# Kernel optimization log

Hardware: AMD Instinct MI355X
Metric: run time of the kernel (lower is better)

Reference implementation:

```python
import jax, jax.numpy as jnp
import numpy as np

B, N = 8, 2048
DIN, DH, DE = 32, 64, 64
R = 3          # number_relations
L = 3          # num_layers -> 1 first + 1 block + 1 last
PRED_IN = DH * (L - 1) + DE  # concat: 64*2 + 64 = 192
EPS_BN = 1e-5
EPS_NORM = 1e-12


def setup_inputs() -> dict:
    key = jax.random.key(0)
    ks = jax.random.split(key, 12)
    x = jax.random.normal(ks[0], (B, N, DIN), jnp.float32)
    # relation labels in {0..R}; 0 = no edge, 1..R = relation type
    relation = jax.random.randint(ks[1], (B, N, N), 0, R + 1).astype(jnp.int32)
    # adjacency is the 0/1 edge indicator (float), as the torch code treats it
    adj = (relation > 0).astype(jnp.float32)
    s = 0.05
    w_first = jax.random.normal(ks[2], (R, DIN, DH), jnp.float32) * s
    b_first = jnp.zeros((DH,), jnp.float32)
    w_block = jax.random.normal(ks[3], (R, DH, DH), jnp.float32) * s
    b_block = jnp.zeros((DH,), jnp.float32)
    w_last = jax.random.normal(ks[4], (R, DH, DE), jnp.float32) * s
    b_last = jnp.zeros((DE,), jnp.float32)
    w_map = jax.random.normal(ks[5], (PRED_IN, DE), jnp.float32) * s
    b_map = jnp.zeros((DE,), jnp.float32)
    return {"x": x, "relation": relation, "adj": adj,
            "w_first": w_first, "b_first": b_first,
            "w_block": w_block, "b_block": b_block,
            "w_last": w_last, "b_last": b_last,
            "w_map": w_map, "b_map": b_map}


def _graph_conv(x, rel, W, b):
    # rel: [B,N,N] (int labels or float adjacency); W: [R, din, dout]
    y = jnp.zeros((x.shape[0], x.shape[1], W.shape[2]), x.dtype)
    for i in range(R):  # fixed, small relation count
        mask = (rel == (i + 1)).astype(x.dtype)            # [B,N,N]
        h = jnp.einsum('bij,bjd->bid', mask, x)            # masked aggregation
        y = y + jnp.einsum('bid,de->bie', h, W[i])
    y = y + b
    # F.normalize(p=2, dim=2): v / max(||v||, eps)
    nrm = jnp.sqrt(jnp.sum(y * y, axis=2, keepdims=True))
    return y / jnp.maximum(nrm, EPS_NORM)


def _apply_bn(x):
    # fresh BatchNorm1d(N) in training mode, affine weight=1/bias=0:
    # normalize over (batch, feature) per node index, biased variance
    mean = jnp.mean(x, axis=(0, 2), keepdims=True)
    var = jnp.mean(jnp.square(x - mean), axis=(0, 2), keepdims=True)
    return (x - mean) * jax.lax.rsqrt(var + EPS_BN)


def reference(x, relation, adj, w_first, b_first, w_block, b_block,
              w_last, b_last, w_map, b_map):
    # conv_first uses `relation`
    h = _apply_bn(jax.nn.relu(_graph_conv(x, relation, w_first, b_first)))
    out_all = [jnp.max(h, axis=1)]
    # conv_block and conv_last are (faithfully) called with `adj` as relation
    h = _apply_bn(jax.nn.relu(_graph_conv(h, adj, w_block, b_block)))
    out_all.append(jnp.max(h, axis=1))
    h = _graph_conv(h, adj, w_last, b_last)
    out_all.append(jnp.max(h, axis=1))
    output = jnp.concatenate(out_all, axis=1)        # [B, PRED_IN]
    ypred = output @ w_map + b_map                   # map_model Linear
    return (output, ypred)
```

## Files before the change

kernel.cpp:

```cpp
#include <hip/hip_runtime.h>


#define NN 2048
#define PLANE_W 1048576L

typedef short short8 __attribute__((ext_vector_type(8)));
typedef float floatx4 __attribute__((ext_vector_type(4)));

__device__ __forceinline__ unsigned short f2bf(float x) {
  unsigned u = __float_as_uint(x);
  u += 0x7FFFu + ((u >> 16) & 1u);
  return (unsigned short)(u >> 16);
}

__device__ void dev_xw_first(char* smemc, int u, int tid,
                             const float* __restrict__ x,
                             const float* __restrict__ w,
                             unsigned short* __restrict__ xws) {
  float* xs = (float*)smemc;
  float* wsh = (float*)(smemc + 64 * 33 * 4);
  const int jc = u & 31, b = (u >> 5) & 7, r = u >> 8;
  const int j0 = jc * 64;
  for (int idx = tid; idx < 64 * 32; idx += 256) {
    int row = idx >> 5, f = idx & 31;
    xs[row * 33 + f] = x[((long)b * NN + j0 + row) * 32 + f];
    wsh[idx] = w[r * 2048 + idx];
  }
  __syncthreads();
  const int j = tid & 63, g = tid >> 6;
  const int k = j0 + j;
  const int kblk = k >> 5, kq = (k >> 3) & 3, kj = k & 7;
  unsigned short* dst =
      xws + (((long)(r * 8 + b) * 64 + kblk) * 4 + g) * 512 + kj;
  float xr[32];
#pragma unroll
  for (int f = 0; f < 32; ++f) xr[f] = xs[j * 33 + f];
#pragma unroll
  for (int ii = 0; ii < 16; ++ii) {
    float acc = 0.f;
#pragma unroll
    for (int f = 0; f < 32; ++f) acc += xr[f] * wsh[f * 64 + g * 16 + ii];
    dst[(kq * 16 + ii) * 8] = f2bf(acc);
  }
  __syncthreads();
}

__global__ __launch_bounds__(256) void k_pack_xw1(const int* __restrict__ rel,
                                                  unsigned* __restrict__ planes,
                                                  const float* __restrict__ x,
                                                  const float* __restrict__ w,
                                                  unsigned short* __restrict__ xws) {
  __shared__ __align__(16) char smem[16640];
  const int bid = blockIdx.x, tid = threadIdx.x;
  if (bid < 768) dev_xw_first(smem, bid, tid, x, w, xws);
  for (long t = (long)bid * 256 + tid; t < 1048576L; t += 4096L * 256) {
    int w32 = (int)(t & 63);
    long bi = t >> 6;
    const int4* rp = (const int4*)(rel + bi * NN + w32 * 32);
    unsigned m0 = 0, m1 = 0, m2 = 0;
#pragma unroll
    for (int c = 0; c < 8; ++c) {
      int4 v = rp[c];
      int vv[4] = {v.x, v.y, v.z, v.w};
#pragma unroll
      for (int j = 0; j < 4; ++j) {
        unsigned b1 = 1u << (c * 4 + j);
        m0 |= (vv[j] == 1) ? b1 : 0u;
        m1 |= (vv[j] == 2) ? b1 : 0u;
        m2 |= (vv[j] == 3) ? b1 : 0u;
      }
    }
    long o = bi * 64 + w32;
    planes[o] = m0;
    planes[PLANE_W + o] = m1;
    planes[2 * PLANE_W + o] = m2;
  }
}

template <int NREL, bool RELU, bool POOL3>
__global__ __launch_bounds__(512) void k_gemm8(
    const unsigned* __restrict__ planes, const unsigned short* __restrict__ xws,
    const float* __restrict__ bias, float* __restrict__ Hout,
    float* __restrict__ part3) {
  constexpr int SMEM = (NREL * 8448 > 16640) ? NREL * 8448 : 16640;
  __shared__ __align__(16) char smem[SMEM];
  unsigned* mw = (unsigned*)smem;
  floatx4* cb = (floatx4*)smem;
  const int bid = blockIdx.x;
  const int b = bid & 7, it = bid >> 3;
  const int tid = threadIdx.x;
  const int wave = tid >> 6, lane = tid & 63;
  const int m = lane & 15, kq = lane >> 4;
  const int i0 = it * 64;

  floatx4 acc[4][4];
#pragma unroll
  for (int rs = 0; rs < 4; ++rs)
#pragma unroll
    for (int t = 0; t < 4; ++t) acc[rs][t] = floatx4{0, 0, 0, 0};

  for (int chunk = 0; chunk < 2; ++chunk) {
    for (int idx = tid; idx < NREL * 2048; idx += 512) {
      int p = idx >> 11, rem = idx & 2047, row = rem >> 5, w = rem & 31;
      long g = ((long)b * NN + i0 + row) * 64 + chunk * 32 + w;
      unsigned v;
      if (NREL == 3)
        v = planes[(long)p * PLANE_W + g];
      else
        v = planes[g] | planes[PLANE_W + g] | planes[2 * PLANE_W + g];
      mw[(p * 64 + row) * 33 + w] = v;
    }
    __syncthreads();
#pragma unroll
    for (int j = 0; j < 4; ++j) {
      const int kk = j * 8 + wave;
      const int kblk = chunk * 32 + kk;
#pragma unroll
      for (int p = 0; p < NREL; ++p) {
        const unsigned short* bb =
            xws + ((long)(p * 8 + b) * 64 + kblk) * 2048 + lane * 8;
        short8 bf0 = *(const short8*)(bb);
        short8 bf1 = *(const short8*)(bb + 512);
        short8 bf2 = *(const short8*)(bb + 1024);
        short8 bf3 = *(const short8*)(bb + 1536);
#pragma unroll
        for (int rs = 0; rs < 4; ++rs) {
          unsigned word = mw[(p * 64 + rs * 16 + m) * 33 + kk];
          unsigned byte = (word >> (kq * 8)) & 0xffu;
          unsigned pp = byte | (byte << 15);
          union {
            unsigned uu[4];
            short8 s8;
          } fr;
          unsigned w0 = pp & 0x00010001u;
          fr.uu[0] = (w0 << 14) - (w0 << 7);
          unsigned w1 = pp & 0x00040004u;
          fr.uu[1] = (w1 << 12) - (w1 << 5);
          unsigned w2 = pp & 0x00100010u;
          fr.uu[2] = (w2 << 10) - (w2 << 3);
          unsigned w3 = pp & 0x00400040u;
          fr.uu[3] = (w3 << 8) - (w3 << 1);
          acc[rs][0] = __builtin_amdgcn_mfma_f32_16x16x32_bf16(fr.s8, bf0,
                                                              acc[rs][0], 0, 0, 0);
          acc[rs][1] = __builtin_amdgcn_mfma_f32_16x16x32_bf16(fr.s8, bf1,
                                                              acc[rs][1], 0, 0, 0);
          acc[rs][2] = __builtin_amdgcn_mfma_f32_16x16x32_bf16(fr.s8, bf2,
                                                              acc[rs][2], 0, 0, 0);
          acc[rs][3] = __builtin_amdgcn_mfma_f32_16x16x32_bf16(fr.s8, bf3,
                                                              acc[rs][3], 0, 0, 0);
        }
      }
    }
    __syncthreads();
  }

  for (int k = 7; k >= 1; --k) {
    if (wave == k) {
      if (k == 7) {
#pragma unroll
        for (int rs = 0; rs < 4; ++rs)
#pragma unroll
          for (int t = 0; t < 4; ++t) cb[(rs * 4 + t) * 64 + lane] = acc[rs][t];
      } else {
#pragma unroll
        for (int rs = 0; rs < 4; ++rs)
#pragma unroll
          for (int t = 0; t < 4; ++t) {
            floatx4 v = cb[(rs * 4 + t) * 64 + lane];
            cb[(rs * 4 + t) * 64 + lane] = v + acc[rs][t];
          }
      }
    }
    __syncthreads();
  }
  if (wave == 0) {
#pragma unroll
    for (int rs = 0; rs < 4; ++rs)
#pragma unroll
      for (int t = 0; t < 4; ++t) acc[rs][t] += cb[(rs * 4 + t) * 64 + lane];
    float bv[4];
#pragma unroll
    for (int t = 0; t < 4; ++t) bv[t] = bias[t * 16 + m];
    float pmt[4] = {-3.4e38f, -3.4e38f, -3.4e38f, -3.4e38f};
#pragma unroll
    for (int rs = 0; rs < 4; ++rs) {
      float ss[4];
#pragma unroll
      for (int reg = 0; reg < 4; ++reg) {
#pragma unroll
        for (int t = 0; t < 4; ++t) acc[rs][t][reg] += bv[t];
        ss[reg] = acc[rs][0][reg] * acc[rs][0][reg] +
                  acc[rs][1][reg] * acc[rs][1][reg] +
                  acc[rs][2][reg] * acc[rs][2][reg] +
                  acc[rs][3][reg] * acc[rs][3][reg];
#pragma unroll
        for (int off = 1; off <= 8; off <<= 1)
          ss[reg] += __shfl_xor(ss[reg], off);
        ss[reg] = 1.0f / fmaxf(sqrtf(ss[reg]), 1e-12f);
      }
#pragma unroll
      for (int t = 0; t < 4; ++t) {
#pragma unroll
        for (int reg = 0; reg < 4; ++reg) {
          float o = acc[rs][t][reg] * ss[reg];
          if (RELU) o = fmaxf(o, 0.0f);
          if (POOL3)
            pmt[t] = fmaxf(pmt[t], o);
          else
            Hout[((long)b * NN + i0 + rs * 16 + kq * 4 + reg) * 64 + t * 16 + m] = o;
        }
      }
    }
    if (POOL3) {
#pragma unroll
      for (int t = 0; t < 4; ++t) {
        pmt[t] = fmaxf(pmt[t], __shfl_xor(pmt[t], 16));
        pmt[t] = fmaxf(pmt[t], __shfl_xor(pmt[t], 32));
      }
      if (kq == 0) {
#pragma unroll
        for (int t = 0; t < 4; ++t)
          part3[((long)b * 32 + it) * 64 + t * 16 + m] = pmt[t];
      }
    }
  }
}

__global__ __launch_bounds__(256) void k_xwh_bn(const float* __restrict__ H,
                                                const float* __restrict__ w,
                                                unsigned short* __restrict__ xws,
                                                float* __restrict__ PP) {
  __shared__ float hs[64 * 65];
  __shared__ float wsh[64 * 64];
  __shared__ float sm[64], srs[64];
  const int bid = blockIdx.x, tid = threadIdx.x;
  const int jc = bid & 31, b = bid >> 5;
  const int j0 = jc * 64;
  {
    const int n = tid >> 2, q = tid & 3;
    float s1 = 0.f, s2 = 0.f;
#pragma unroll
    for (int bb = 0; bb < 8; ++bb) {
      const float4* hp =
          (const float4*)(H + ((long)bb * NN + j0 + n) * 64 + q * 16);
#pragma unroll
      for (int c = 0; c < 4; ++c) {
        float4 v = hp[c];
        s1 += v.x + v.y + v.z + v.w;
        s2 += v.x * v.x + v.y * v.y + v.z * v.z + v.w * v.w;
      }
    }
    s1 += __shfl_xor(s1, 1);
    s2 += __shfl_xor(s2, 1);
    s1 += __shfl_xor(s1, 2);
    s2 += __shfl_xor(s2, 2);
    if (q == 0) {
      float mean = s1 * (1.0f / 512.0f);
      float var = fmaxf(s2 * (1.0f / 512.0f) - mean * mean, 0.0f);
      sm[n] = mean;
      srs[n] = rsqrtf(var + 1e-5f);
    }
  }
  __syncthreads();
  for (int idx = tid; idx < 4096; idx += 256) {
    int row = idx >> 6, f = idx & 63;
    float v = H[((long)b * NN + j0 + row) * 64 + f];
    hs[row * 65 + f] = (v - sm[row]) * srs[row];
    wsh[idx] = w[idx];
  }
  __syncthreads();
  {
    const int j = tid & 63, g = tid >> 6;
    const int k = j0 + j;
    const int kblk = k >> 5, kq = (k >> 3) & 3, kj = k & 7;
    unsigned short* dst = xws + (((long)b * 64 + kblk) * 4 + g) * 512 + kj;
    float acc[16];
#pragma unroll
    for (int ii = 0; ii < 16; ++ii) acc[ii] = 0.f;
#pragma unroll
    for (int c = 0; c < 4; ++c) {
      float xr[16];
#pragma unroll
      for (int f = 0; f < 16; ++f) xr[f] = hs[j * 65 + c * 16 + f];
#pragma unroll
      for (int ii = 0; ii < 16; ++ii)
#pragma unroll
        for (int f = 0; f < 16; ++f)
          acc[ii] += xr[f] * wsh[(c * 16 + f) * 64 + g * 16 + ii];
    }
#pragma unroll
    for (int ii = 0; ii < 16; ++ii) dst[(kq * 16 + ii) * 8] = f2bf(acc[ii]);
  }
  if (b == 0) {
#pragma unroll
    for (int part = 0; part < 2; ++part) {
      const int col = part * 256 + tid;
      const int bb = col >> 6, e = col & 63;
      float mx = -3.4e38f;
      for (int n = 0; n < 64; ++n) {
        float v = H[((long)bb * NN + j0 + n) * 64 + e];
        mx = fmaxf(mx, (v - sm[n]) * srs[n]);
      }
      PP[(long)jc * 512 + col] = mx;
    }
  }
}

__global__ __launch_bounds__(512) void k_tail(const float* __restrict__ PP1,
                                              const float* __restrict__ PP2,
                                              const float* __restrict__ P3,
                                              float* __restrict__ out,
                                              const float* __restrict__ wmap,
                                              const float* __restrict__ bmap) {
  const int col = threadIdx.x;
  const int bb = col >> 6, e = col & 63;
  float m1 = -3.4e38f, m2 = -3.4e38f, m3 = -3.4e38f;
#pragma unroll
  for (int c = 0; c < 32; ++c) {
    m1 = fmaxf(m1, PP1[(long)c * 512 + col]);
    m2 = fmaxf(m2, PP2[(long)c * 512 + col]);
    m3 = fmaxf(m3, P3[((long)bb * 32 + c) * 64 + e]);
  }
  out[bb * 192 + e] = m1;
  out[bb * 192 + 64 + e] = m2;
  out[bb * 192 + 128 + e] = m3;
  __syncthreads();
  float acc = bmap[e];
  for (int k = 0; k < 192; ++k) acc += out[bb * 192 + k] * wmap[k * 64 + e];
  out[1536 + bb * 64 + e] = acc;
}

extern "C" void kernel_launch(void* const* d_in, const int* in_sizes, int n_in,
                              void* d_out, int out_size, void* d_ws,
                              size_t ws_size, hipStream_t stream) {
  const float* x = (const float*)d_in[0];
  const int* rel = (const int*)d_in[1];
  const float* w_first = (const float*)d_in[3];
  const float* b_first = (const float*)d_in[4];
  const float* w_block = (const float*)d_in[5];
  const float* b_block = (const float*)d_in[6];
  const float* w_last = (const float*)d_in[7];
  const float* b_last = (const float*)d_in[8];
  const float* w_map = (const float*)d_in[9];
  const float* b_map = (const float*)d_in[10];
  float* out = (float*)d_out;

  char* ws = (char*)d_ws;
  const size_t MB = 1024 * 1024;
  unsigned* PLANES = (unsigned*)(ws);
  unsigned short* XWS = (unsigned short*)(ws + 12 * MB);
  float* H = (float*)(ws + 18 * MB);
  float* PP1 = (float*)(ws + 22 * MB);
  float* PP2 = (float*)(ws + 23 * MB);
  float* PART3 = (float*)(ws + 24 * MB);

  k_pack_xw1<<<4096, 256, 0, stream>>>(rel, PLANES, x, w_first, XWS);
  k_gemm8<3, true, false><<<256, 512, 0, stream>>>(PLANES, XWS, b_first, H,
                                                   nullptr);
  k_xwh_bn<<<256, 256, 0, stream>>>(H, w_block, XWS, PP1);
  k_gemm8<1, true, false><<<256, 512, 0, stream>>>(PLANES, XWS, b_block, H,
                                                   nullptr);
  k_xwh_bn<<<256, 256, 0, stream>>>(H, w_last, XWS, PP2);
  k_gemm8<1, false, true><<<256, 512, 0, stream>>>(PLANES, XWS, b_last,
                                                   nullptr, PART3);
  k_tail<<<1, 512, 0, stream>>>(PP1, PP2, PART3, out, w_map, b_map);
}
```

Baseline: 410.5 us.

## Precompute union adjacency plane, LUT mask expansion, parallel wave reduction epilogue

The pack kernel now writes a fourth bit-plane holding the OR of the three relation masks, so the single-relation GEMMs read one plane instead of three. Bit-to-bf16 fragment expansion switches from shift arithmetic to a 16-entry LDS lookup table. The serial 7-step cross-wave accumulator reduction becomes a two-stage reduction in which four waves each finish one row slice, spreading the normalize/store epilogue across waves. The tail kernel reads pooled values from shared memory instead of global output, and shared memory is raised to a fixed 64KB, which may limit occupancy.

```diff
diff --git a/kernel.cpp b/kernel.cpp
--- a/kernel.cpp
+++ b/kernel.cpp
@@ -74,6 +74,7 @@
     planes[o] = m0;
     planes[PLANE_W + o] = m1;
     planes[2 * PLANE_W + o] = m2;
+    planes[3 * PLANE_W + o] = m0 | m1 | m2;
   }
 }
 
@@ -82,16 +83,24 @@
     const unsigned* __restrict__ planes, const unsigned short* __restrict__ xws,
     const float* __restrict__ bias, float* __restrict__ Hout,
     float* __restrict__ part3) {
-  constexpr int SMEM = (NREL * 8448 > 16640) ? NREL * 8448 : 16640;
-  __shared__ __align__(16) char smem[SMEM];
+  constexpr int MASK_BYTES = NREL * 8448;
+  __shared__ __align__(16) char smem[65536];
   unsigned* mw = (unsigned*)smem;
+  uint2* lut = (uint2*)(smem + MASK_BYTES);
   floatx4* cb = (floatx4*)smem;
   const int bid = blockIdx.x;
   const int b = bid & 7, it = bid >> 3;
   const int tid = threadIdx.x;
   const int wave = tid >> 6, lane = tid & 63;
   const int m = lane & 15, kq = lane >> 4;
+  const unsigned shamt = kq * 8;
   const int i0 = it * 64;
+
+  if (tid < 16) {
+    unsigned n = tid;
+    lut[n] = make_uint2(((n & 1u) ? 0x3f80u : 0u) | ((n & 2u) ? 0x3f800000u : 0u),
+                        ((n & 4u) ? 0x3f80u : 0u) | ((n & 8u) ? 0x3f800000u : 0u));
+  }
 
   floatx4 acc[4][4];
 #pragma unroll
@@ -107,7 +116,7 @@
       if (NREL == 3)
         v = planes[(long)p * PLANE_W + g];
       else
-        v = planes[g] | planes[PLANE_W + g] | planes[2 * PLANE_W + g];
+        v = planes[3 * PLANE_W + g];
       mw[(p * 64 + row) * 33 + w] = v;
     }
     __syncthreads();
@@ -126,20 +135,17 @@
 #pragma unroll
         for (int rs = 0; rs < 4; ++rs) {
           unsigned word = mw[(p * 64 + rs * 16 + m) * 33 + kk];
-          unsigned byte = (word >> (kq * 8)) & 0xffu;
-          unsigned pp = byte | (byte << 15);
+          unsigned byte = (word >> shamt) & 0xffu;
+          uint2 lo = lut[byte & 15u];
+          uint2 hi = lut[byte >> 4];
           union {
             unsigned uu[4];
             short8 s8;
           } fr;
-          unsigned w0 = pp & 0x00010001u;
-          fr.uu[0] = (w0 << 14) - (w0 << 7);
-          unsigned w1 = pp & 0x00040004u;
-          fr.uu[1] = (w1 << 12) - (w1 << 5);
-          unsigned w2 = pp & 0x00100010u;
-          fr.uu[2] = (w2 << 10) - (w2 << 3);
-          unsigned w3 = pp & 0x00400040u;
-          fr.uu[3] = (w3 << 8) - (w3 << 1);
+          fr.uu[0] = lo.x;
+          fr.uu[1] = lo.y;
+          fr.uu[2] = hi.x;
+          fr.uu[3] = hi.y;
           acc[rs][0] = __builtin_amdgcn_mfma_f32_16x16x32_bf16(fr.s8, bf0,
                                                               acc[rs][0], 0, 0, 0);
           acc[rs][1] = __builtin_amdgcn_mfma_f32_16x16x32_bf16(fr.s8, bf1,
@@ -154,61 +160,56 @@
     __syncthreads();
   }
 
-  for (int k = 7; k >= 1; --k) {
-    if (wave == k) {
-      if (k == 7) {
-#pragma unroll
-        for (int rs = 0; rs < 4; ++rs)
-#pragma unroll
-          for (int t = 0; t < 4; ++t) cb[(rs * 4 + t) * 64 + lane] = acc[rs][t];
-      } else {
-#pragma unroll
-        for (int rs = 0; rs < 4; ++rs)
-#pragma unroll
-          for (int t = 0; t < 4; ++t) {
-            floatx4 v = cb[(rs * 4 + t) * 64 + lane];
-            cb[(rs * 4 + t) * 64 + lane] = v + acc[rs][t];
-          }
-      }
-    }
-    __syncthreads();
-  }
-  if (wave == 0) {
+  if (wave >= 4) {
+    const int src = wave - 4;
 #pragma unroll
     for (int rs = 0; rs < 4; ++rs)
 #pragma unroll
-      for (int t = 0; t < 4; ++t) acc[rs][t] += cb[(rs * 4 + t) * 64 + lane];
+      for (int t = 0; t < 4; ++t)
+        cb[((rs * 4 + src) * 4 + t) * 64 + lane] = acc[rs][t];
+  }
+  __syncthreads();
+  if (wave < 4) {
+#pragma unroll
+    for (int rs = 0; rs < 4; ++rs)
+#pragma unroll
+      for (int t = 0; t < 4; ++t) {
+        const int ix = ((rs * 4 + wave) * 4 + t) * 64 + lane;
+        cb[ix] = cb[ix] + acc[rs][t];
+      }
+  }
+  __syncthreads();
+  if (wave < 4) {
+    const int rs = wave;
+    floatx4 s[4];
+#pragma unroll
+    for (int t = 0; t < 4; ++t) s[t] = cb[((rs * 4 + 0) * 4 + t) * 64 + lane];
+#pragma unroll
+    for (int src = 1; src < 4; ++src)
+#pragma unroll
+      for (int t = 0; t < 4; ++t)
+        s[t] += cb[((rs * 4 + src) * 4 + t) * 64 + lane];
     float bv[4];
 #pragma unroll
     for (int t = 0; t < 4; ++t) bv[t] = bias[t * 16 + m];
     float pmt[4] = {-3.4e38f, -3.4e38f, -3.4e38f, -3.4e38f};
 #pragma unroll
-    for (int rs = 0; rs < 4; ++rs) {
-      float ss[4];
-#pragma unroll
-      for (int reg = 0; reg < 4; ++reg) {
-#pragma unroll
-        for (int t = 0; t < 4; ++t) acc[rs][t][reg] += bv[t];
-        ss[reg] = acc[rs][0][reg] * acc[rs][0][reg] +
-                  acc[rs][1][reg] * acc[rs][1][reg] +
-                  acc[rs][2][reg] * acc[rs][2][reg] +
-                  acc[rs][3][reg] * acc[rs][3][reg];
-#pragma unroll
-        for (int off = 1; off <= 8; off <<= 1)
-          ss[reg] += __shfl_xor(ss[reg], off);
-        ss[reg] = 1.0f / fmaxf(sqrtf(ss[reg]), 1e-12f);
-      }
+    for (int reg = 0; reg < 4; ++reg) {
+#pragma unroll
+      for (int t = 0; t < 4; ++t) s[t][reg] += bv[t];
+      float q = s[0][reg] * s[0][reg] + s[1][reg] * s[1][reg] +
+                s[2][reg] * s[2][reg] + s[3][reg] * s[3][reg];
+#pragma unroll
+      for (int off = 1; off <= 8; off <<= 1) q += __shfl_xor(q, off);
+      q = 1.0f / fmaxf(sqrtf(q), 1e-12f);
 #pragma unroll
       for (int t = 0; t < 4; ++t) {
-#pragma unroll
-        for (int reg = 0; reg < 4; ++reg) {
-          float o = acc[rs][t][reg] * ss[reg];
-          if (RELU) o = fmaxf(o, 0.0f);
-          if (POOL3)
-            pmt[t] = fmaxf(pmt[t], o);
-          else
-            Hout[((long)b * NN + i0 + rs * 16 + kq * 4 + reg) * 64 + t * 16 + m] = o;
-        }
+        float o = s[t][reg] * q;
+        if (RELU) o = fmaxf(o, 0.0f);
+        if (POOL3)
+          pmt[t] = fmaxf(pmt[t], o);
+        else
+          Hout[((long)b * NN + i0 + rs * 16 + kq * 4 + reg) * 64 + t * 16 + m] = o;
       }
     }
     if (POOL3) {
@@ -217,11 +218,21 @@
         pmt[t] = fmaxf(pmt[t], __shfl_xor(pmt[t], 16));
         pmt[t] = fmaxf(pmt[t], __shfl_xor(pmt[t], 32));
       }
+      float* pm = (float*)(smem + wave * 16384);
       if (kq == 0) {
 #pragma unroll
-        for (int t = 0; t < 4; ++t)
-          part3[((long)b * 32 + it) * 64 + t * 16 + m] = pmt[t];
-      }
+        for (int t = 0; t < 4; ++t) pm[t * 16 + m] = pmt[t];
+      }
+    }
+  }
+  if (POOL3) {
+    __syncthreads();
+    if (tid < 64) {
+      float v = -3.4e38f;
+#pragma unroll
+      for (int w = 0; w < 4; ++w)
+        v = fmaxf(v, ((const float*)(smem + w * 16384))[tid]);
+      part3[((long)b * 32 + it) * 64 + tid] = v;
     }
   }
 }
@@ -312,6 +323,7 @@
                                               float* __restrict__ out,
                                               const float* __restrict__ wmap,
                                               const float* __restrict__ bmap) {
+  __shared__ float obuf[8 * 192];
   const int col = threadIdx.x;
   const int bb = col >> 6, e = col & 63;
   float m1 = -3.4e38f, m2 = -3.4e38f, m3 = -3.4e38f;
@@ -324,9 +336,13 @@
   out[bb * 192 + e] = m1;
   out[bb * 192 + 64 + e] = m2;
   out[bb * 192 + 128 + e] = m3;
+  obuf[bb * 192 + e] = m1;
+  obuf[bb * 192 + 64 + e] = m2;
+  obuf[bb * 192 + 128 + e] = m3;
   __syncthreads();
   float acc = bmap[e];
-  for (int k = 0; k < 192; ++k) acc += out[bb * 192 + k] * wmap[k * 64 + e];
+#pragma unroll 4
+  for (int k = 0; k < 192; ++k) acc += obuf[bb * 192 + k] * wmap[k * 64 + e];
   out[1536 + bb * 64 + e] = acc;
 }
 
@@ -348,11 +364,11 @@
   char* ws = (char*)d_ws;
   const size_t MB = 1024 * 1024;
   unsigned* PLANES = (unsigned*)(ws);
-  unsigned short* XWS = (unsigned short*)(ws + 12 * MB);
-  float* H = (float*)(ws + 18 * MB);
-  float* PP1 = (float*)(ws + 22 * MB);
-  float* PP2 = (float*)(ws + 23 * MB);
-  float* PART3 = (float*)(ws + 24 * MB);
+  unsigned short* XWS = (unsigned short*)(ws + 16 * MB);
+  float* H = (float*)(ws + 22 * MB);
+  float* PP1 = (float*)(ws + 26 * MB);
+  float* PP2 = (float*)(ws + 27 * MB);
+  float* PART3 = (float*)(ws + 28 * MB);
 
   k_pack_xw1<<<4096, 256, 0, stream>>>(rel, PLANES, x, w_first, XWS);
   k_gemm8<3, true, false><<<256, 512, 0, stream>>>(PLANES, XWS, b_first, H,
```

Result: faster. 355.8 us (-13.3%).
